# Kernel optimization log

Hardware: AMD Instinct MI355X
Metric: run time of the kernel (lower is better)

## Reference

```python
import jax, jax.numpy as jnp
import numpy as np

TOKENS = 16384
IN_F = 2048
OUT_F = 2048
RANK = 32
GROUP = 64          # int4 scale group size
PAD = 256           # token padding multiple used by the fused activation quantizer
QMAX = 7.0          # signed int4 symmetric quantization


def setup_inputs() -> dict:
    key = jax.random.key(0)
    ks = jax.random.split(key, 7)
    x = jax.random.normal(ks[0], (TOKENS, IN_F), dtype=jnp.float32)
    # packed int4 weights: two signed nibbles per int8 lane
    qweight = jax.random.randint(ks[1], (OUT_F, IN_F // 2), -128, 128, dtype=jnp.int8)
    # per-group weight scales [in//group, out], strictly positive
    wscales = jnp.abs(jax.random.normal(ks[2], (IN_F // GROUP, OUT_F), dtype=jnp.float32)) * 0.01 + 1e-4
    # activation smoothing factors, positive and near 1
    smooth_factor = jnp.abs(jax.random.normal(ks[3], (IN_F,), dtype=jnp.float32)) * 0.5 + 0.75
    bias = jax.random.normal(ks[4], (OUT_F,), dtype=jnp.float32) * 0.01
    proj_down = jax.random.normal(ks[5], (IN_F, RANK), dtype=jnp.float32) * 0.02
    proj_up = jax.random.normal(ks[6], (OUT_F, RANK), dtype=jnp.float32) * 0.02
    return {"x": x, "qweight": qweight, "wscales": wscales,
            "smooth_factor": smooth_factor, "bias": bias,
            "proj_down": proj_down, "proj_up": proj_up}


def _unpack_int4(qweight):
    # low nibble = even input channel, high nibble = odd input channel; arithmetic shifts keep sign
    low = jnp.right_shift(jnp.left_shift(qweight, 4), 4)
    high = jnpp = jnp.right_shift(qweight, 4)
    w = jnp.stack([low, high], axis=-1).reshape(qweight.shape[0], qweight.shape[1] * 2)
    return w.astype(jnp.float32)  # [out, in], values in [-8, 7]


def _forward(x, qweight, wscales, smooth_factor, bias, proj_down, proj_up):
    T = x.shape[0]
    t_pad = ((T + PAD - 1) // PAD) * PAD
    # activation smoothing
    xs = x / smooth_factor
    xs_p = jnp.pad(xs, ((0, t_pad - T), (0, 0)))
    # per-token per-64-group symmetric int4 activation quantization
    xg = xs_p.reshape(t_pad, IN_F // GROUP, GROUP)
    amax = jnp.max(jnp.abs(xg), axis=-1)                       # [Tp, G]
    ascales = jnp.where(amax > 0, amax / QMAX, jnp.float32(1.0))
    qx = jnp.clip(jnp.round(xg / ascales[..., None]), -8.0, 7.0)
    xdq = (qx * ascales[..., None]).reshape(t_pad, IN_F)       # dequantized activations
    # dequantize packed int4 weights with per-group scales
    w = _unpack_int4(qweight)                                  # [out, in]
    wdq = (w.reshape(OUT_F, IN_F // GROUP, GROUP) * wscales.T[:, :, None]).reshape(OUT_F, IN_F)
    # packed GEMM (dequantized equivalent) + fused low-rank residual + bias
    y = xdq @ wdq.T                                            # [Tp, out]
    y = y + (xs_p @ proj_down) @ proj_up.T + bias
    return y[:T]


def reference(x, qweight, wscales, smooth_factor, bias, proj_down, proj_up):
    return _forward(x, qweight, wscales, smooth_factor, bias, proj_down, proj_up)
```

## Files before the change

### kernel.cpp

```cpp
#include <hip/hip_runtime.h>

#define TOKENS 16384
#define INF 2048
#define OUTF 2048
#define NGROUP 32
#define RANK 32
#define BM 128
#define BN 128

typedef int   int32x4  __attribute__((ext_vector_type(4)));
typedef int   int32x2  __attribute__((ext_vector_type(2)));
typedef float floatx4  __attribute__((ext_vector_type(4)));
typedef short bf16x8   __attribute__((ext_vector_type(8)));

typedef __attribute__((address_space(1))) const void gconst_t;
typedef __attribute__((address_space(3))) void ldsv_t;

__device__ __forceinline__ void gload_lds16(const void* g, void* l) {
  __builtin_amdgcn_global_load_lds((gconst_t*)g, (ldsv_t*)l, 16, 0, 0);
}

__device__ __forceinline__ unsigned short f2bf(float f) {
  unsigned u = __float_as_uint(f);
  unsigned r = (u + 0x7FFFu + ((u >> 16) & 1u)) >> 16;
  return (unsigned short)r;
}

__device__ __forceinline__ unsigned unp2(int e0, int e1) {
  int l0 = ((int)((unsigned)e0 << 28)) >> 28;
  int h0 = ((int)((unsigned)e0 << 24)) >> 28;
  int l1 = ((int)((unsigned)e1 << 28)) >> 28;
  int h1 = ((int)((unsigned)e1 << 24)) >> 28;
  return (l0 & 0xFF) | ((h0 & 0xFF) << 8) | ((l1 & 0xFF) << 16) | ((h1 & 0xFF) << 24);
}

__global__ __launch_bounds__(256) void unpack_kernel(const int* __restrict__ qw,
                                                     signed char* __restrict__ wq8) {
  int idx = blockIdx.x * 256 + threadIdx.x;
  const int4* src = (const int4*)qw;
  int4 v0 = src[idx * 2 + 0];
  int4 v1 = src[idx * 2 + 1];
  int4 out;
  out.x = (int)unp2(v0.x, v0.y);
  out.y = (int)unp2(v0.z, v0.w);
  out.z = (int)unp2(v1.x, v1.y);
  out.w = (int)unp2(v1.z, v1.w);
  *(int4*)(wq8 + (size_t)idx * 16) = out;
}

__global__ __launch_bounds__(256) void prep_pdT(const float* __restrict__ pd,
                                                unsigned short* __restrict__ pdT) {
  int idx = blockIdx.x * 256 + threadIdx.x;
  int r = idx >> 11, c = idx & 2047;
  pdT[idx] = f2bf(pd[(size_t)c * RANK + r]);
}

__global__ __launch_bounds__(256) void quant_kernel(
    const float* __restrict__ x, const float* __restrict__ smooth,
    const unsigned short* __restrict__ pdT,
    signed char* __restrict__ qx8, float* __restrict__ ascales,
    float* __restrict__ tdown) {
  __shared__ char lds[32768];
  int tid = threadIdx.x, lane = tid & 63, wid = tid >> 6;
  int t0 = blockIdx.x * 32;
  int mi = wid >> 1, ni = wid & 1;
  floatx4 acc = {0.f, 0.f, 0.f, 0.f};

  floatx4 xv[8];
  floatx4 sm;
  int32x4 pv[4];

  auto issue_loads = [&](int kc) {
    const float* xb = x + (size_t)(t0 + wid * 8) * INF + kc * 256 + lane * 4;
#pragma unroll
    for (int r = 0; r < 8; ++r) xv[r] = *(const floatx4*)(xb + r * INF);
    sm = *(const floatx4*)(smooth + kc * 256 + lane * 4);
#pragma unroll
    for (int q = 0; q < 4; ++q) {
      int flat = tid + q * 256;
      int row = flat >> 5, c16 = flat & 31;
      pv[q] = *(const int32x4*)((const char*)pdT + (size_t)row * 4096 + kc * 512 + c16 * 16);
    }
  };

  issue_loads(0);

  for (int kc = 0; kc < 8; ++kc) {
    floatx4 rsm;
    rsm[0] = 1.0f / sm[0]; rsm[1] = 1.0f / sm[1];
    rsm[2] = 1.0f / sm[2]; rsm[3] = 1.0f / sm[3];
#pragma unroll
    for (int q = 0; q < 4; ++q) {
      int flat = tid + q * 256;
      int row = flat >> 5, c16 = flat & 31;
      int byte = (row * 512 + c16 * 16) ^ ((row & 7) << 4);
      *(int32x4*)(lds + 16384 + byte) = pv[q];
    }
#pragma unroll
    for (int r = 0; r < 8; ++r) {
      floatx4 xs;
      xs[0] = xv[r][0] * rsm[0]; xs[1] = xv[r][1] * rsm[1];
      xs[2] = xv[r][2] * rsm[2]; xs[3] = xv[r][3] * rsm[3];
      float m4 = fmaxf(fmaxf(fabsf(xs[0]), fabsf(xs[1])),
                       fmaxf(fabsf(xs[2]), fabsf(xs[3])));
      m4 = fmaxf(m4, __shfl_xor(m4, 1, 64));
      m4 = fmaxf(m4, __shfl_xor(m4, 2, 64));
      m4 = fmaxf(m4, __shfl_xor(m4, 4, 64));
      m4 = fmaxf(m4, __shfl_xor(m4, 8, 64));
      float ascale = m4 > 0.f ? m4 / 7.0f : 1.0f;
      float rq = 1.0f / ascale;
      int tok = t0 + wid * 8 + r;
      if ((lane & 15) == 0)
        ascales[(size_t)tok * NGROUP + kc * 4 + (lane >> 4)] = ascale;
      int pk = 0;
#pragma unroll
      for (int b = 0; b < 4; ++b) {
        float qf = fminf(7.f, fmaxf(-8.f, rintf(xs[b] * rq)));
        pk |= ((int)qf & 0xFF) << (8 * b);
      }
      *(int*)(qx8 + (size_t)tok * INF + kc * 256 + lane * 4) = pk;
      unsigned lo = (unsigned)f2bf(xs[0]) | ((unsigned)f2bf(xs[1]) << 16);
      unsigned hi = (unsigned)f2bf(xs[2]) | ((unsigned)f2bf(xs[3]) << 16);
      int lrow = wid * 8 + r;
      int xbyte = (lrow * 512 + lane * 8) ^ ((lrow & 7) << 4);
      int32x2 wv; wv[0] = (int)lo; wv[1] = (int)hi;
      *(int32x2*)(lds + xbyte) = wv;
    }
    __syncthreads();
    if (kc + 1 < 8) issue_loads(kc + 1);
#pragma unroll
    for (int ks = 0; ks < 8; ++ks) {
      int arow = mi * 16 + (lane & 15);
      int ab = (arow * 512 + ks * 64 + ((lane >> 4) << 4)) ^ ((arow & 7) << 4);
      bf16x8 av = *(const bf16x8*)(lds + ab);
      int brow = ni * 16 + (lane & 15);
      int bb = (brow * 512 + ks * 64 + ((lane >> 4) << 4)) ^ ((brow & 7) << 4);
      bf16x8 bv = *(const bf16x8*)(lds + 16384 + bb);
      acc = __builtin_amdgcn_mfma_f32_16x16x32_bf16(av, bv, acc, 0, 0, 0);
    }
    __syncthreads();
  }

  int trow = t0 + mi * 16 + ((lane >> 4) << 2);
  int col = ni * 16 + (lane & 15);
#pragma unroll
  for (int r = 0; r < 4; ++r)
    tdown[(size_t)(trow + r) * RANK + col] = acc[r];
}

__global__ __launch_bounds__(256, 2) void gemm_kernel(
    const signed char* __restrict__ qx8, const signed char* __restrict__ wq8,
    const float* __restrict__ ascales, const float* __restrict__ wscales,
    const float* __restrict__ tdown, const float* __restrict__ pu,
    const float* __restrict__ bias, float* __restrict__ y) {
  __shared__ char smem[65536];
  signed char* a_lds = (signed char*)smem;
  signed char* b_lds = (signed char*)(smem + 16384);
  float* as_t = (float*)(smem + 32768);
  float* ws_t = (float*)(smem + 49152);

  int tid = threadIdx.x;
  int lane = tid & 63;
  int wid = tid >> 6;
  int wr = wid >> 1, wc = wid & 1;
  int o0 = blockIdx.x * BN;
  int t0 = blockIdx.y * BM;

  {
    int tt = tid >> 1, h = (tid & 1) * 16;
    const float* src = ascales + (size_t)(t0 + tt) * NGROUP + h;
#pragma unroll
    for (int q = 0; q < 4; ++q) {
      float4 v = *(const float4*)(src + q * 4);
      as_t[(h + q * 4 + 0) * BM + tt] = v.x;
      as_t[(h + q * 4 + 1) * BM + tt] = v.y;
      as_t[(h + q * 4 + 2) * BM + tt] = v.z;
      as_t[(h + q * 4 + 3) * BM + tt] = v.w;
    }
    int gg = tid >> 3, cc = (tid & 7) * 16;
    const float* src2 = wscales + (size_t)gg * OUTF + o0 + cc;
#pragma unroll
    for (int q = 0; q < 4; ++q)
      *(float4*)&ws_t[gg * BN + cc + q * 4] = *(const float4*)(src2 + q * 4);
  }

  float acc[4][4][4];
#pragma unroll
  for (int m = 0; m < 4; ++m)
#pragma unroll
    for (int n = 0; n < 4; ++n)
#pragma unroll
      for (int r = 0; r < 4; ++r) acc[m][n][r] = 0.f;

  auto stage = [&](int buf, int g) {
#pragma unroll
    for (int i = 0; i < 2; ++i) {
      int c = tid + i * 256;
      const signed char* ga = qx8 + (size_t)(t0 + (c >> 2)) * INF + g * 64 + (c & 3) * 16;
      gload_lds16(ga, a_lds + buf * 8192 + (wid + i * 4) * 1024);
      const signed char* gb = wq8 + (size_t)(o0 + (c >> 2)) * INF + g * 64 + (c & 3) * 16;
      gload_lds16(gb, b_lds + buf * 8192 + (wid + i * 4) * 1024);
    }
  };

  stage(0, 0);
  __syncthreads();

  for (int g = 0; g < NGROUP; ++g) {
    int buf = g & 1;
    if (g + 1 < NGROUP) stage(buf ^ 1, g + 1);

    int koff = (lane >> 4) << 4;
    int32x4 af[4], bf_[4];
#pragma unroll
    for (int m = 0; m < 4; ++m)
      af[m] = *(const int32x4*)(a_lds + buf * 8192 +
                                ((wr << 6) + (m << 4) + (lane & 15)) * 64 + koff);
#pragma unroll
    for (int n = 0; n < 4; ++n)
      bf_[n] = *(const int32x4*)(b_lds + buf * 8192 +
                                 ((wc << 6) + (n << 4) + (lane & 15)) * 64 + koff);

    float asv[4][4];
#pragma unroll
    for (int m = 0; m < 4; ++m) {
      floatx4 v = *(const floatx4*)&as_t[g * BM + (wr << 6) + (m << 4) + ((lane >> 4) << 2)];
      asv[m][0] = v[0]; asv[m][1] = v[1]; asv[m][2] = v[2]; asv[m][3] = v[3];
    }
    float wsv[4];
#pragma unroll
    for (int n = 0; n < 4; ++n) wsv[n] = ws_t[g * BN + (wc << 6) + (n << 4) + (lane & 15)];

#pragma unroll
    for (int m = 0; m < 4; ++m)
#pragma unroll
      for (int n = 0; n < 4; ++n) {
        int32x4 zero = {0, 0, 0, 0};
        int32x4 d = __builtin_amdgcn_mfma_i32_16x16x64_i8(af[m], bf_[n], zero, 0, 0, 0);
#pragma unroll
        for (int r = 0; r < 4; ++r)
          acc[m][n][r] += (float)d[r] * (asv[m][r] * wsv[n]);
      }
    __syncthreads();
  }

  unsigned short* td_lds = (unsigned short*)smem;
  unsigned short* pu_lds = (unsigned short*)(smem + 8192);
  {
    int row = tid >> 1, h = (tid & 1) * 16;
    const float* ts = tdown + (size_t)(t0 + row) * RANK + h;
    const float* ps = pu + (size_t)(o0 + row) * RANK + h;
    unsigned tw[8], pw[8];
#pragma unroll
    for (int q = 0; q < 4; ++q) {
      float4 v = *(const float4*)(ts + q * 4);
      tw[q * 2 + 0] = (unsigned)f2bf(v.x) | ((unsigned)f2bf(v.y) << 16);
      tw[q * 2 + 1] = (unsigned)f2bf(v.z) | ((unsigned)f2bf(v.w) << 16);
      float4 p = *(const float4*)(ps + q * 4);
      pw[q * 2 + 0] = (unsigned)f2bf(p.x) | ((unsigned)f2bf(p.y) << 16);
      pw[q * 2 + 1] = (unsigned)f2bf(p.z) | ((unsigned)f2bf(p.w) << 16);
    }
    int4 s0, s1;
    s0.x = (int)tw[0]; s0.y = (int)tw[1]; s0.z = (int)tw[2]; s0.w = (int)tw[3];
    s1.x = (int)tw[4]; s1.y = (int)tw[5]; s1.z = (int)tw[6]; s1.w = (int)tw[7];
    *(int4*)(td_lds + row * 32 + h) = s0;
    *(int4*)(td_lds + row * 32 + h + 8) = s1;
    s0.x = (int)pw[0]; s0.y = (int)pw[1]; s0.z = (int)pw[2]; s0.w = (int)pw[3];
    s1.x = (int)pw[4]; s1.y = (int)pw[5]; s1.z = (int)pw[6]; s1.w = (int)pw[7];
    *(int4*)(pu_lds + row * 32 + h) = s0;
    *(int4*)(pu_lds + row * 32 + h + 8) = s1;
  }
  __syncthreads();

  bf16x8 ta[4], pb4[4];
  int koff8 = (lane >> 4) << 3;
#pragma unroll
  for (int m = 0; m < 4; ++m)
    ta[m] = *(const bf16x8*)&td_lds[((wr << 6) + (m << 4) + (lane & 15)) * 32 + koff8];
#pragma unroll
  for (int n = 0; n < 4; ++n)
    pb4[n] = *(const bf16x8*)&pu_lds[((wc << 6) + (n << 4) + (lane & 15)) * 32 + koff8];

#pragma unroll
  for (int n = 0; n < 4; ++n) {
    int oc = o0 + (wc << 6) + (n << 4) + (lane & 15);
    float bv = bias[oc];
#pragma unroll
    for (int m = 0; m < 4; ++m) {
      floatx4 c;
      c[0] = acc[m][n][0]; c[1] = acc[m][n][1]; c[2] = acc[m][n][2]; c[3] = acc[m][n][3];
      c = __builtin_amdgcn_mfma_f32_16x16x32_bf16(ta[m], pb4[n], c, 0, 0, 0);
#pragma unroll
      for (int r = 0; r < 4; ++r) {
        int tr = t0 + (wr << 6) + (m << 4) + ((lane >> 4) << 2) + r;
        y[(size_t)tr * OUTF + oc] = c[r] + bv;
      }
    }
  }
}

extern "C" void kernel_launch(void* const* d_in, const int* in_sizes, int n_in,
                              void* d_out, int out_size, void* d_ws, size_t ws_size,
                              hipStream_t stream) {
  const float* x      = (const float*)d_in[0];
  const int*   qw     = (const int*)d_in[1];
  const float* wsc    = (const float*)d_in[2];
  const float* smooth = (const float*)d_in[3];
  const float* bias   = (const float*)d_in[4];
  const float* pd     = (const float*)d_in[5];
  const float* pu     = (const float*)d_in[6];
  float* y = (float*)d_out;

  char* ws = (char*)d_ws;
  signed char* qx8 = (signed char*)ws;
  signed char* wq8 = (signed char*)(ws + 33554432);
  float* ascales   = (float*)(ws + 33554432 + 4194304);
  float* tdown     = (float*)(ws + 33554432 + 4194304 + 2097152);
  unsigned short* pdT = (unsigned short*)((char*)d_out + (64u << 20));

  unpack_kernel<<<1024, 256, 0, stream>>>(qw, wq8);
  prep_pdT<<<256, 256, 0, stream>>>(pd, pdT);
  quant_kernel<<<TOKENS / 32, 256, 0, stream>>>(x, smooth, pdT, qx8, ascales, tdown);
  gemm_kernel<<<dim3(OUTF / BN, TOKENS / BM), 256, 0, stream>>>(
      qx8, wq8, ascales, wsc, tdown, pu, bias, y);
}
```

Baseline: 209.8 us.

## Triple-buffer int8 GEMM LDS tiles with XOR swizzle and single barrier per step

Moves the int8 GEMM main loop from double to triple buffering in LDS, prefetching two groups ahead and using explicit vmcnt waits plus one barrier per iteration instead of two. It also XOR-swizzles the 16-byte chunks of each A/B row to cut LDS bank conflicts on fragment reads, precomputes the fragment offsets, and raises wave priority around the MFMA block. LDS use grows from 64KB to 80KB, which may limit occupancy to fewer blocks per CU. The scale multiply is also reassociated, which can change rounding slightly.

Result: no change. 206.6 us (-1.5%).

```diff
diff --git a/kernel.cpp b/kernel.cpp
--- a/kernel.cpp
+++ b/kernel.cpp
@@ -153,11 +153,9 @@
     const float* __restrict__ ascales, const float* __restrict__ wscales,
     const float* __restrict__ tdown, const float* __restrict__ pu,
     const float* __restrict__ bias, float* __restrict__ y) {
-  __shared__ char smem[65536];
-  signed char* a_lds = (signed char*)smem;
-  signed char* b_lds = (signed char*)(smem + 16384);
-  float* as_t = (float*)(smem + 32768);
-  float* ws_t = (float*)(smem + 49152);
+  __shared__ char smem[81920];
+  float* as_t = (float*)(smem + 49152);
+  float* ws_t = (float*)(smem + 65536);
 
   int tid = threadIdx.x;
   int lane = tid & 63;
@@ -192,45 +190,61 @@
 #pragma unroll
       for (int r = 0; r < 4; ++r) acc[m][n][r] = 0.f;
 
-  auto stage = [&](int buf, int g) {
+  auto stage = [&](int g) {
+    int bufb = (g % 3) * 16384;
 #pragma unroll
     for (int i = 0; i < 2; ++i) {
       int c = tid + i * 256;
-      const signed char* ga = qx8 + (size_t)(t0 + (c >> 2)) * INF + g * 64 + (c & 3) * 16;
-      gload_lds16(ga, a_lds + buf * 8192 + (wid + i * 4) * 1024);
-      const signed char* gb = wq8 + (size_t)(o0 + (c >> 2)) * INF + g * 64 + (c & 3) * 16;
-      gload_lds16(gb, b_lds + buf * 8192 + (wid + i * 4) * 1024);
+      int row = c >> 2;
+      int l = (c & 3) ^ ((row >> 1) & 3);
+      gload_lds16(qx8 + (size_t)(t0 + row) * INF + g * 64 + l * 16,
+                  smem + bufb + (wid + i * 4) * 1024);
+      gload_lds16(wq8 + (size_t)(o0 + row) * INF + g * 64 + l * 16,
+                  smem + bufb + 8192 + (wid + i * 4) * 1024);
     }
   };
 
-  stage(0, 0);
+  int aoff[4], boff[4];
+#pragma unroll
+  for (int m = 0; m < 4; ++m) {
+    int arow = (wr << 6) + (m << 4) + (lane & 15);
+    aoff[m] = arow * 64 + ((((lane >> 4)) ^ ((arow >> 1) & 3)) << 4);
+    int brow = (wc << 6) + (m << 4) + (lane & 15);
+    boff[m] = 8192 + brow * 64 + ((((lane >> 4)) ^ ((brow >> 1) & 3)) << 4);
+  }
+  int asoff = (wr << 6) + ((lane >> 4) << 2);
+  int wsoff = (wc << 6) + (lane & 15);
+
   __syncthreads();
+  stage(0);
+  stage(1);
 
   for (int g = 0; g < NGROUP; ++g) {
-    int buf = g & 1;
-    if (g + 1 < NGROUP) stage(buf ^ 1, g + 1);
-
-    int koff = (lane >> 4) << 4;
+    if (g == NGROUP - 1) asm volatile("s_waitcnt vmcnt(0)" ::: "memory");
+    else                 asm volatile("s_waitcnt vmcnt(4)" ::: "memory");
+    __builtin_amdgcn_s_barrier();
+    __builtin_amdgcn_sched_barrier(0);
+
+    if (g + 2 < NGROUP) stage(g + 2);
+
+    int bufb = (g % 3) * 16384;
     int32x4 af[4], bf_[4];
 #pragma unroll
-    for (int m = 0; m < 4; ++m)
-      af[m] = *(const int32x4*)(a_lds + buf * 8192 +
-                                ((wr << 6) + (m << 4) + (lane & 15)) * 64 + koff);
-#pragma unroll
-    for (int n = 0; n < 4; ++n)
-      bf_[n] = *(const int32x4*)(b_lds + buf * 8192 +
-                                 ((wc << 6) + (n << 4) + (lane & 15)) * 64 + koff);
+    for (int m = 0; m < 4; ++m) af[m] = *(const int32x4*)(smem + bufb + aoff[m]);
+#pragma unroll
+    for (int n = 0; n < 4; ++n) bf_[n] = *(const int32x4*)(smem + bufb + boff[n]);
 
     float asv[4][4];
 #pragma unroll
     for (int m = 0; m < 4; ++m) {
-      floatx4 v = *(const floatx4*)&as_t[g * BM + (wr << 6) + (m << 4) + ((lane >> 4) << 2)];
+      floatx4 v = *(const floatx4*)&as_t[g * BM + asoff + (m << 4)];
       asv[m][0] = v[0]; asv[m][1] = v[1]; asv[m][2] = v[2]; asv[m][3] = v[3];
     }
     float wsv[4];
 #pragma unroll
-    for (int n = 0; n < 4; ++n) wsv[n] = ws_t[g * BN + (wc << 6) + (n << 4) + (lane & 15)];
-
+    for (int n = 0; n < 4; ++n) wsv[n] = ws_t[g * BN + wsoff + (n << 4)];
+
+    __builtin_amdgcn_s_setprio(1);
 #pragma unroll
     for (int m = 0; m < 4; ++m)
 #pragma unroll
@@ -239,10 +253,12 @@
         int32x4 d = __builtin_amdgcn_mfma_i32_16x16x64_i8(af[m], bf_[n], zero, 0, 0, 0);
 #pragma unroll
         for (int r = 0; r < 4; ++r)
-          acc[m][n][r] += (float)d[r] * (asv[m][r] * wsv[n]);
+          acc[m][n][r] += ((float)d[r] * wsv[n]) * asv[m][r];
       }
-    __syncthreads();
-  }
+    __builtin_amdgcn_s_setprio(0);
+  }
+
+  __syncthreads();
 
   unsigned short* td_lds = (unsigned short*)smem;
   unsigned short* pu_lds = (unsigned short*)(smem + 8192);
```
